# Kernel optimization log

Measured on AMD Instinct MI355X. Metric: run time of the kernel, lower is better.

The kernel has to match this reference:

```python
import jax, jax.numpy as jnp
import numpy as np

B, N, T = 64, 512, 2048  # batch, max text len, max mel len


def setup_inputs() -> dict:
    key = jax.random.key(0)
    k1, k2, k3 = jax.random.split(key, 3)
    A = jax.random.uniform(k1, (B, N, T), dtype=jnp.float32)
    g = jnp.float32(0.2)
    mel_lens = jax.random.randint(k2, (B,), T // 2, T + 1)   # t (valid mel frames)
    seq_lens = jax.random.randint(k3, (B,), N // 2, N + 1)   # n (valid text tokens)
    return {"A": A, "g": g, "mel_lens": mel_lens, "seq_lens": seq_lens}


def reference(A, g, mel_lens, seq_lens):
    # Vectorized equivalent of the per-sample loop:
    # W[i, :n_i, :t_i] = 1 - exp(-(j/n_i - k/t_i)^2 / (2 g^2)), zero elsewhere.
    dt = A.dtype
    n_idx = jnp.arange(N)                                   # text axis index j
    t_idx = jnp.arange(T)                                   # mel  axis index k
    n_len = seq_lens[:, None, None]                          # [B,1,1]
    t_len = mel_lens[:, None, None]                          # [B,1,1]
    n = n_idx[None, :, None].astype(dt) / n_len.astype(dt)   # [B,N,1]
    t = t_idx[None, None, :].astype(dt) / t_len.astype(dt)   # [B,1,T]
    diff = n - t                                             # [B,N,T]
    w = 1.0 - jnp.exp(-(diff * diff) / (2.0 * g * g))
    mask = (n_idx[None, :, None] < n_len) & (t_idx[None, None, :] < t_len)
    W = jnp.where(mask, w, jnp.zeros((), dt))
    # (W * A).mean(dim=0).sum() == sum(W * A) / B
    return jnp.sum(W * A) / A.shape[0]
```

## Files before the change

### kernel.cpp

```cpp
#include <hip/hip_runtime.h>


#define GAL_B 64
#define GAL_N 512
#define GAL_T 2048

__global__ __launch_bounds__(256) void gal_main(
    const float* __restrict__ A,
    const float* __restrict__ gptr,
    const int*   __restrict__ mel_lens,
    const int*   __restrict__ seq_lens,
    float*       __restrict__ partials)
{
    const int row = blockIdx.x;
    const int b   = row >> 9;
    const int n   = row & (GAL_N - 1);
    const int seq = seq_lens[b];

    float local = 0.0f;
    if (n < seq) {
        const int   mel     = mel_lens[b];
        const float g       = gptr[0];
        const float inv2g2  = 1.0f / (2.0f * g * g);
        const float nf      = (float)n / (float)seq;
        const float inv_mel = 1.0f / (float)mel;
        const float4* Arow  = (const float4*)(A + ((size_t)row << 11));
        const int nvec = (mel + 3) >> 2;
        for (int j = threadIdx.x; j < nvec; j += 256) {
            float4 a = Arow[j];
            const int t0 = j << 2;
            {
                float d = nf - (float)(t0 + 0) * inv_mel;
                float w = 1.0f - __expf(-d * d * inv2g2);
                local += (t0 + 0 < mel) ? w * a.x : 0.0f;
            }
            {
                float d = nf - (float)(t0 + 1) * inv_mel;
                float w = 1.0f - __expf(-d * d * inv2g2);
                local += (t0 + 1 < mel) ? w * a.y : 0.0f;
            }
            {
                float d = nf - (float)(t0 + 2) * inv_mel;
                float w = 1.0f - __expf(-d * d * inv2g2);
                local += (t0 + 2 < mel) ? w * a.z : 0.0f;
            }
            {
                float d = nf - (float)(t0 + 3) * inv_mel;
                float w = 1.0f - __expf(-d * d * inv2g2);
                local += (t0 + 3 < mel) ? w * a.w : 0.0f;
            }
        }
    }

    #pragma unroll
    for (int off = 32; off > 0; off >>= 1)
        local += __shfl_down(local, off, 64);

    __shared__ float s[4];
    const int lane = threadIdx.x & 63;
    const int wave = threadIdx.x >> 6;
    if (lane == 0) s[wave] = local;
    __syncthreads();
    if (threadIdx.x == 0)
        partials[blockIdx.x] = (s[0] + s[1]) + (s[2] + s[3]);
}

__global__ __launch_bounds__(256) void gal_reduce(
    const float* __restrict__ partials, int n, float* __restrict__ out)
{
    const float4* p4 = (const float4*)partials;
    const int nv = n >> 2;
    float local = 0.0f;
    for (int i = threadIdx.x; i < nv; i += 256) {
        float4 v = p4[i];
        local += (v.x + v.y) + (v.z + v.w);
    }
    #pragma unroll
    for (int off = 32; off > 0; off >>= 1)
        local += __shfl_down(local, off, 64);
    __shared__ float s[4];
    if ((threadIdx.x & 63) == 0) s[threadIdx.x >> 6] = local;
    __syncthreads();
    if (threadIdx.x == 0)
        out[0] = ((s[0] + s[1]) + (s[2] + s[3])) * (1.0f / (float)GAL_B);
}

extern "C" void kernel_launch(void* const* d_in, const int* in_sizes, int n_in,
                              void* d_out, int out_size, void* d_ws, size_t ws_size,
                              hipStream_t stream) {
    const float* A        = (const float*)d_in[0];
    const float* g        = (const float*)d_in[1];
    const int*   mel_lens = (const int*)d_in[2];
    const int*   seq_lens = (const int*)d_in[3];
    float* out      = (float*)d_out;
    float* partials = (float*)d_ws;

    const int nrows = GAL_B * GAL_N;
    gal_main<<<nrows, 256, 0, stream>>>(A, g, mel_lens, seq_lens, partials);
    gal_reduce<<<1, 256, 0, stream>>>(partials, nrows, out);
}
```

Measured before the change: 337.4 us.

## Fuse reduction into grid-stride kernel with atomic accumulation

Replaces the one-block-per-row main kernel and separate single-block reduce with a persistent grid-stride kernel of 2048 blocks. Per-batch lengths and reciprocals are cached in shared memory, and each block atomically adds its scaled sum into the output after a memset. This removes the second launch and the partials round trip, and cuts the block count. In exchange it adds a memset, float atomics with order-dependent rounding, and possible load imbalance from the fixed row striding.

Result: slower. 346.2 us (+2.6%).

```diff
diff --git a/kernel.cpp b/kernel.cpp
--- a/kernel.cpp
+++ b/kernel.cpp
@@ -4,30 +4,49 @@
 #define GAL_B 64
 #define GAL_N 512
 #define GAL_T 2048
+#define GAL_GRID 2048
 
-__global__ __launch_bounds__(256) void gal_main(
+__global__ __launch_bounds__(256) void gal_fused(
     const float* __restrict__ A,
     const float* __restrict__ gptr,
     const int*   __restrict__ mel_lens,
     const int*   __restrict__ seq_lens,
-    float*       __restrict__ partials)
+    float*       __restrict__ out)
 {
-    const int row = blockIdx.x;
-    const int b   = row >> 9;
-    const int n   = row & (GAL_N - 1);
-    const int seq = seq_lens[b];
+    __shared__ float s_inv_seq[GAL_B];
+    __shared__ float s_inv_mel[GAL_B];
+    __shared__ int   s_seq[GAL_B];
+    __shared__ int   s_mel[GAL_B];
+
+    if (threadIdx.x < GAL_B) {
+        const int sq = seq_lens[threadIdx.x];
+        const int ml = mel_lens[threadIdx.x];
+        s_seq[threadIdx.x]     = sq;
+        s_mel[threadIdx.x]     = ml;
+        s_inv_seq[threadIdx.x] = 1.0f / (float)sq;
+        s_inv_mel[threadIdx.x] = 1.0f / (float)ml;
+    }
+    __syncthreads();
+
+    const float g      = gptr[0];
+    const float inv2g2 = 1.0f / (2.0f * g * g);
 
     float local = 0.0f;
-    if (n < seq) {
-        const int   mel     = mel_lens[b];
-        const float g       = gptr[0];
-        const float inv2g2  = 1.0f / (2.0f * g * g);
-        const float nf      = (float)n / (float)seq;
-        const float inv_mel = 1.0f / (float)mel;
+
+    for (int row = blockIdx.x; row < GAL_B * GAL_N; row += GAL_GRID) {
+        const int b = row >> 9;
+        const int n = row & (GAL_N - 1);
+        const int seq = s_seq[b];
+        if (n >= seq) continue;
+
+        const int   mel     = s_mel[b];
+        const float nf      = (float)n * s_inv_seq[b];
+        const float inv_mel = s_inv_mel[b];
         const float4* Arow  = (const float4*)(A + ((size_t)row << 11));
         const int nvec = (mel + 3) >> 2;
+
         for (int j = threadIdx.x; j < nvec; j += 256) {
-            float4 a = Arow[j];
+            const float4 a = Arow[j];
             const int t0 = j << 2;
             {
                 float d = nf - (float)(t0 + 0) * inv_mel;
@@ -56,33 +75,15 @@
     for (int off = 32; off > 0; off >>= 1)
         local += __shfl_down(local, off, 64);
 
-    __shared__ float s[4];
+    __shared__ float s_red[4];
     const int lane = threadIdx.x & 63;
     const int wave = threadIdx.x >> 6;
-    if (lane == 0) s[wave] = local;
+    if (lane == 0) s_red[wave] = local;
     __syncthreads();
-    if (threadIdx.x == 0)
-        partials[blockIdx.x] = (s[0] + s[1]) + (s[2] + s[3]);
-}
-
-__global__ __launch_bounds__(256) void gal_reduce(
-    const float* __restrict__ partials, int n, float* __restrict__ out)
-{
-    const float4* p4 = (const float4*)partials;
-    const int nv = n >> 2;
-    float local = 0.0f;
-    for (int i = threadIdx.x; i < nv; i += 256) {
-        float4 v = p4[i];
-        local += (v.x + v.y) + (v.z + v.w);
+    if (threadIdx.x == 0) {
+        const float blocksum = (s_red[0] + s_red[1]) + (s_red[2] + s_red[3]);
+        atomicAdd(out, blocksum * (1.0f / (float)GAL_B));
     }
-    #pragma unroll
-    for (int off = 32; off > 0; off >>= 1)
-        local += __shfl_down(local, off, 64);
-    __shared__ float s[4];
-    if ((threadIdx.x & 63) == 0) s[threadIdx.x >> 6] = local;
-    __syncthreads();
-    if (threadIdx.x == 0)
-        out[0] = ((s[0] + s[1]) + (s[2] + s[3])) * (1.0f / (float)GAL_B);
 }
 
 extern "C" void kernel_launch(void* const* d_in, const int* in_sizes, int n_in,
@@ -92,10 +93,8 @@
     const float* g        = (const float*)d_in[1];
     const int*   mel_lens = (const int*)d_in[2];
     const int*   seq_lens = (const int*)d_in[3];
-    float* out      = (float*)d_out;
-    float* partials = (float*)d_ws;
+    float* out = (float*)d_out;
 
-    const int nrows = GAL_B * GAL_N;
-    gal_main<<<nrows, 256, 0, stream>>>(A, g, mel_lens, seq_lens, partials);
-    gal_reduce<<<1, 256, 0, stream>>>(partials, nrows, out);
+    hipMemsetAsync(out, 0, sizeof(float) * (size_t)out_size, stream);
+    gal_fused<<<GAL_GRID, 256, 0, stream>>>(A, g, mel_lens, seq_lens, out);
 }
```
